# Kernel optimization log

Hardware: AMD Instinct MI355X
Metric: run time of the kernel (lower is better)

The kernel has to match this reference:

```python
import jax, jax.numpy as jnp
import numpy as np

NUM_HEADS = 4
NUM_EXPERTS = 8
TOP_K = 2
AUX_W = 0.1


def setup_inputs() -> dict:
    key = jax.random.key(0)
    ks = jax.random.split(key, 16)
    B, W, C, T = 32, 64, 27, 2000
    E_EEG, H, S = 200, 256, 768
    D2 = 2 * H  # MoE input/hidden dim = 512
    s = 0.02

    def p(k, shape):
        return (jax.random.normal(k, shape, jnp.float32) * s)

    z = lambda *shape: jnp.zeros(shape, jnp.float32)
    return {
        "eeg_windows": jax.random.normal(ks[0], (B, W, C, T), jnp.float32),
        "padding_mask": jnp.zeros((B, W), bool),
        "smiles_emb": jax.random.normal(ks[1], (B, S), jnp.float32),
        # window encoder (linear stand-in): flatten (C*T) -> E_EEG
        "enc_W": p(ks[2], (C * T, E_EEG)), "enc_b": z(E_EEG),
        # aggregator (masked-mean + linear stand-in): E_EEG -> H
        "agg_W": p(ks[3], (E_EEG, H)), "agg_b": z(H),
        # smiles projection
        "smiles_W": p(ks[4], (S, H)), "smiles_b": z(H),
        # cross attention
        "Wq": p(ks[5], (H, H)), "bq": z(H),
        "Wk": p(ks[6], (H, H)), "bk": z(H),
        "Wv": p(ks[7], (H, H)), "bv": z(H),
        "Wo": p(ks[8], (H, H)), "bo": z(H),
        # MoE gate + experts
        "gate_W": p(ks[9], (D2, NUM_EXPERTS)), "gate_b": z(NUM_EXPERTS),
        "exp_W1": p(ks[10], (NUM_EXPERTS, D2, D2)), "exp_b1": z(NUM_EXPERTS, D2),
        "exp_W2": p(ks[11], (NUM_EXPERTS, D2, H)), "exp_b2": z(NUM_EXPERTS, H),
        # classifier
        "ln_g": jnp.ones((H,), jnp.float32), "ln_b": z(H),
        "cls_W": p(ks[12], (H, 2)), "cls_b": z(2),
    }


def reference(eeg_windows, padding_mask, smiles_emb, enc_W, enc_b, agg_W, agg_b,
              smiles_W, smiles_b, Wq, bq, Wk, bk, Wv, bv, Wo, bo,
              gate_W, gate_b, exp_W1, exp_b1, exp_W2, exp_b2,
              ln_g, ln_b, cls_W, cls_b):
    B, W, C, T = eeg_windows.shape
    H = agg_W.shape[1]
    dh = H // NUM_HEADS

    # --- window encoding (stand-in linear encoder) ---
    wemb = eeg_windows.reshape(B, W, C * T) @ enc_W + enc_b  # (B, W, E_EEG)

    # --- aggregator: masked mean pool over windows, then project ---
    valid = (~padding_mask).astype(wemb.dtype)[..., None]      # (B, W, 1)
    pooled = (wemb * valid).sum(1) / jnp.maximum(valid.sum(1), 1.0)
    eeg_emb = pooled @ agg_W + agg_b                           # (B, H)

    smiles_proj = smiles_emb @ smiles_W + smiles_b             # (B, H)

    # --- cross attention (single query token over single kv token) ---
    q = (eeg_emb @ Wq + bq).reshape(B, NUM_HEADS, dh)
    k = (smiles_proj @ Wk + bk).reshape(B, NUM_HEADS, dh)
    v = (smiles_proj @ Wv + bv).reshape(B, NUM_HEADS, dh)
    scores = (q * k).sum(-1, keepdims=True) / jnp.sqrt(jnp.float32(dh))
    attn = jnp.exp(scores - scores)  # softmax over a single key == 1
    attended = (attn * v).reshape(B, H) @ Wo + bo              # (B, H)

    fused = jnp.concatenate([attended, smiles_proj], axis=-1)  # (B, 2H)

    # --- sparse MoE: dense experts, top-k gate, gather, combine ---
    gate_probs = jax.nn.softmax(fused @ gate_W + gate_b, axis=-1)  # (B, E)
    topk_p, topk_i = jax.lax.top_k(gate_probs, TOP_K)
    topk_p = topk_p / topk_p.sum(-1, keepdims=True)
    h1 = jax.nn.gelu(jnp.einsum('bd,edh->beh', fused, exp_W1) + exp_b1,
                     approximate=False)
    expert_out = jnp.einsum('beh,eho->beo', h1, exp_W2) + exp_b2   # (B, E, H)
    sel = jnp.take_along_axis(expert_out, topk_i[:, :, None], axis=1)
    moe_out = (sel * topk_p[..., None]).sum(1)                     # (B, H)

    usage = gate_probs.mean(0)
    uniform = jnp.ones_like(usage) / usage.shape[-1]
    aux = (usage * jnp.log(uniform) - jnp.log(usage) * uniform).sum()

    # --- classifier: LayerNorm + Linear ---
    mu = moe_out.mean(-1, keepdims=True)
    var = moe_out.var(-1, keepdims=True)
    xn = (moe_out - mu) / jnp.sqrt(var + 1e-5)
    logits = (xn * ln_g + ln_b) @ cls_W + cls_b                    # (B, 2)
    return logits, aux * AUX_W
```

## Files before the change

### kernel.cpp

```cpp
#include <hip/hip_runtime.h>
#include <math.h>

#define HD 256
#define SD 768
#define D2 512
#define NE 8
#define NB 32
#define NBLK 256
#define NTHR 256
#define SFP 516

typedef float f32x4 __attribute__((ext_vector_type(4)));
typedef unsigned u32x4 __attribute__((ext_vector_type(4)));

__device__ __forceinline__ float gelu_exact(float x) {
    return 0.5f * x * (1.0f + erff(x * 0.70710678118654752f));
}

__device__ __forceinline__ void cstf(float* p, float v) {
    __hip_atomic_store(p, v, __ATOMIC_RELAXED, __HIP_MEMORY_SCOPE_AGENT);
}
__device__ __forceinline__ float cldf(const float* p) {
    return __hip_atomic_load(p, __ATOMIC_RELAXED, __HIP_MEMORY_SCOPE_AGENT);
}
__device__ __forceinline__ void csti(int* p, int v) {
    __hip_atomic_store(p, v, __ATOMIC_RELAXED, __HIP_MEMORY_SCOPE_AGENT);
}
__device__ __forceinline__ int cldi(const int* p) {
    return __hip_atomic_load(p, __ATOMIC_RELAXED, __HIP_MEMORY_SCOPE_AGENT);
}

__device__ __forceinline__ void stage16k(const float* __restrict__ gsrc,
                                         float* __restrict__ lds, int t)
{
    const f32x4* src = (const f32x4*)gsrc;
    f32x4 r[16];
    #pragma unroll
    for (int j = 0; j < 16; ++j) {
        const f32x4* p = src + (t + j * 256);
        asm volatile("global_load_dwordx4 %0, %1, off sc0 sc1"
                     : "=v"(r[j]) : "v"(p));
    }
    asm volatile("s_waitcnt vmcnt(0)" ::: "memory");
    __builtin_amdgcn_sched_barrier(0);
    #pragma unroll
    for (int j = 0; j < 16; ++j) {
        int q = t + j * 256;
        *(f32x4*)&lds[(q >> 7) * SFP + (q & 127) * 4] = r[j];
    }
}

__device__ __forceinline__ void post_slot(unsigned* slots, unsigned tok) {
    __syncthreads();
    if (threadIdx.x == 0)
        __hip_atomic_store(slots + blockIdx.x, tok, __ATOMIC_RELAXED,
                           __HIP_MEMORY_SCOPE_AGENT);
}

__device__ __forceinline__ void wait_slots(const unsigned* slots, int nq,
                                           unsigned tok) {
    if (threadIdx.x < 64 && (int)threadIdx.x < nq) {
        const u32x4* p = (const u32x4*)slots + threadIdx.x;
        for (;;) {
            u32x4 v;
            asm volatile("global_load_dwordx4 %0, %1, off sc0 sc1\n\t"
                         "s_waitcnt vmcnt(0)"
                         : "=&v"(v) : "v"(p) : "memory");
            if ((v[0] == tok) & (v[1] == tok) & (v[2] == tok) & (v[3] == tok))
                break;
            __builtin_amdgcn_s_sleep(2);
        }
    }
    __builtin_amdgcn_fence(__ATOMIC_ACQUIRE, "workgroup");
    __syncthreads();
}

#define S_F     0
#define S_W     16512
#define S_R2    (16512 + 8192)
#define S_RED   (16512 + 8192 + 2048)
#define S_SMALL (16512 + 8192 + 2048 + 256)
#define SMEM_F  (16512 + 8192 + 2048 + 256 + 16)

__global__ __launch_bounds__(256) void fused_all(
    const float* __restrict__ smiles,
    const float* __restrict__ sW, const float* __restrict__ sb,
    const float* __restrict__ Wv, const float* __restrict__ bv,
    const float* __restrict__ Wo, const float* __restrict__ bo,
    const float* __restrict__ gW, const float* __restrict__ gb,
    const float* __restrict__ W1, const float* __restrict__ b1,
    const float* __restrict__ W2, const float* __restrict__ b2,
    const float* __restrict__ lng, const float* __restrict__ lnb,
    const float* __restrict__ clsW, const float* __restrict__ clsb,
    float* __restrict__ proj, float* __restrict__ fused,
    float* __restrict__ probs, float* __restrict__ pn,
    int* __restrict__ sel, float* __restrict__ h1,
    float* __restrict__ eo,
    unsigned* __restrict__ slot0, unsigned* __restrict__ slot1,
    unsigned* __restrict__ slot2, unsigned* __restrict__ slot3,
    unsigned* __restrict__ LC, float* __restrict__ out)
{
    __shared__ __align__(16) float smem[SMEM_F];
    __shared__ unsigned s_lc;
    const int bid = blockIdx.x, t = threadIdx.x;

    if (t == 0)
        s_lc = __hip_atomic_load(LC, __ATOMIC_RELAXED, __HIP_MEMORY_SCOPE_AGENT);
    __syncthreads();
    const unsigned tb = s_lc * 2654435761u;

    {
        int r = bid >> 3, sl = bid & 7;
        float* s_in = smem + S_F;
        float* s_red = smem + S_RED;
        const float* srow = smiles + (size_t)r * SD;
        for (int i = t; i < SD / 4; i += NTHR)
            ((float4*)s_in)[i] = ((const float4*)srow)[i];
        __syncthreads();
        int c = t & 31, kq = t >> 5;
        float acc = 0.f;
        const float* wp = sW + (size_t)(kq * 96) * HD + sl * 32 + c;
        #pragma unroll 8
        for (int k = 0; k < 96; ++k)
            acc = fmaf(s_in[kq * 96 + k], wp[(size_t)k * HD], acc);
        s_red[t] = acc;
        __syncthreads();
        if (t < 32) {
            float s = 0.f;
            #pragma unroll
            for (int q = 0; q < 8; ++q) s += s_red[q * 32 + t];
            int col = sl * 32 + t;
            s += sb[col];
            cstf(proj + r * HD + col, s);
            cstf(fused + (size_t)r * 2 * HD + HD + col, s);
        }
    }
    post_slot(slot0, tb + 1u);

    if (bid < NB) {
        wait_slots(slot0 + bid * 8, 2, tb + 1u);
        int b = bid;
        float* s_p   = smem + S_F;
        float* s_v   = smem + S_F + 256;
        float* s_f2  = smem + S_F + 512;
        float* s_acc = smem + S_R2;
        float* s_red = smem + S_RED;
        float* s_gate = smem + S_SMALL;
        s_p[t] = cldf(proj + b * HD + t);
        __syncthreads();
        int ks = t >> 6, cg = t & 63;

        f32x4 av = {0.f, 0.f, 0.f, 0.f};
        #pragma unroll 16
        for (int kk = 0; kk < 64; ++kk) {
            int k = ks * 64 + kk;
            f32x4 w = *(const f32x4*)(Wv + (size_t)k * HD + cg * 4);
            av += s_p[k] * w;
        }
        *(f32x4*)&s_acc[ks * 256 + cg * 4] = av;
        __syncthreads();
        s_v[t] = s_acc[t] + s_acc[256 + t] + s_acc[512 + t] + s_acc[768 + t]
               + bv[t];
        __syncthreads();

        f32x4 ao = {0.f, 0.f, 0.f, 0.f};
        #pragma unroll 16
        for (int kk = 0; kk < 64; ++kk) {
            int k = ks * 64 + kk;
            f32x4 w = *(const f32x4*)(Wo + (size_t)k * HD + cg * 4);
            ao += s_v[k] * w;
        }
        *(f32x4*)&s_acc[ks * 256 + cg * 4] = ao;
        __syncthreads();
        float att = s_acc[t] + s_acc[256 + t] + s_acc[512 + t] + s_acc[768 + t]
                  + bo[t];
        s_f2[t] = att;
        s_f2[HD + t] = s_p[t];
        cstf(fused + (size_t)b * 2 * HD + t, att);
        __syncthreads();

        int e = t & 7, ch = t >> 3;
        float gp = 0.f;
        #pragma unroll
        for (int j = 0; j < 16; ++j) {
            int d = ch * 16 + j;
            gp = fmaf(s_f2[d], gW[d * NE + e], gp);
        }
        s_red[t] = gp;
        __syncthreads();
        for (int off = 128; off >= 8; off >>= 1) {
            if (t < off) s_red[t] += s_red[t + off];
            __syncthreads();
        }
        if (t < NE) s_gate[t] = s_red[t] + gb[t];
        __syncthreads();
        if (t == 0) {
            float m = s_gate[0];
            for (int i = 1; i < NE; ++i) m = fmaxf(m, s_gate[i]);
            float ex[NE], ssum = 0.f;
            for (int i = 0; i < NE; ++i) { ex[i] = expf(s_gate[i] - m); ssum += ex[i]; }
            float pr[NE];
            for (int i = 0; i < NE; ++i) { pr[i] = ex[i] / ssum; cstf(probs + b * NE + i, pr[i]); }
            int i1 = 0;
            for (int i = 1; i < NE; ++i) if (pr[i] > pr[i1]) i1 = i;
            int i2 = (i1 == 0) ? 1 : 0;
            for (int i = 0; i < NE; ++i) if (i != i1 && pr[i] > pr[i2]) i2 = i;
            float p1 = pr[i1], p2 = pr[i2], s12 = p1 + p2;
            csti(sel + b * 2 + 0, i1);
            csti(sel + b * 2 + 1, i2);
            cstf(pn + b * 2 + 0, p1 / s12);
            cstf(pn + b * 2 + 1, p2 / s12);
        }
        post_slot(slot1, tb + 2u);
    }

    wait_slots(slot1, 8, tb + 2u);
    {
        int e = bid >> 5, ct = bid & 31;
        float* s_f  = smem + S_F;
        float* s_w  = smem + S_W;
        float* s_r2 = smem + S_R2;
        stage16k(fused, s_f, t);
        {
            const float* Wb = W1 + (size_t)e * D2 * D2 + ct * 16;
            #pragma unroll
            for (int j = 0; j < 8; ++j) {
                int q = t + j * 256;
                int k = q >> 2, c4 = (q & 3) * 4;
                *(float4*)&s_w[k * 16 + c4] =
                    *(const float4*)(Wb + (size_t)k * D2 + c4);
            }
        }
        __syncthreads();
        int ks = t >> 6, l = t & 63;
        int rp = l >> 2, c4g = l & 3;
        int r0 = rp * 2, r1 = r0 + 1;
        const float* fr0 = s_f + r0 * SFP;
        const float* fr1 = s_f + r1 * SFP;
        const float* wb = s_w + c4g * 4;
        f32x4 a0 = {0.f, 0.f, 0.f, 0.f}, a1 = {0.f, 0.f, 0.f, 0.f};
        #pragma unroll 4
        for (int kq = 0; kq < 32; ++kq) {
            int k = ks * 128 + kq * 4;
            f32x4 w0 = *(const f32x4*)&wb[(k + 0) * 16];
            f32x4 w1 = *(const f32x4*)&wb[(k + 1) * 16];
            f32x4 w2 = *(const f32x4*)&wb[(k + 2) * 16];
            f32x4 w3 = *(const f32x4*)&wb[(k + 3) * 16];
            f32x4 f0 = *(const f32x4*)&fr0[k];
            f32x4 f1 = *(const f32x4*)&fr1[k];
            a0 += f0[0] * w0 + f0[1] * w1 + f0[2] * w2 + f0[3] * w3;
            a1 += f1[0] * w0 + f1[1] * w1 + f1[2] * w2 + f1[3] * w3;
        }
        int cl = c4g * 4;
        #pragma unroll
        for (int j = 0; j < 4; ++j) {
            s_r2[(r0 * 16 + cl + j) * 4 + ks] = a0[j];
            s_r2[(r1 * 16 + cl + j) * 4 + ks] = a1[j];
        }
        __syncthreads();
        #pragma unroll
        for (int o = 0; o < 2; ++o) {
            int outi = t * 2 + o;
            f32x4 p = *(const f32x4*)&s_r2[outi * 4];
            int r = outi >> 4, cl2 = outi & 15;
            int col = ct * 16 + cl2;
            float v = p[0] + p[1] + p[2] + p[3] + b1[e * D2 + col];
            cstf(h1 + ((size_t)e * NB + r) * D2 + col, gelu_exact(v));
        }
    }
    post_slot(slot2, tb + 3u);
    if (bid >= 128) return;

    {
        int e = bid >> 4, ct = bid & 15;
        wait_slots(slot2 + e * 32, 8, tb + 3u);
        float* s_h  = smem + S_F;
        float* s_w  = smem + S_W;
        float* s_r2 = smem + S_R2;
        stage16k(h1 + (size_t)e * NB * D2, s_h, t);
        {
            const float* Wb = W2 + (size_t)e * D2 * HD + ct * 16;
            #pragma unroll
            for (int j = 0; j < 8; ++j) {
                int q = t + j * 256;
                int k = q >> 2, c4 = (q & 3) * 4;
                *(float4*)&s_w[k * 16 + c4] =
                    *(const float4*)(Wb + (size_t)k * HD + c4);
            }
        }
        __syncthreads();
        int ks = t >> 6, l = t & 63;
        int rp = l >> 2, c4g = l & 3;
        int r0 = rp * 2, r1 = r0 + 1;
        const float* fr0 = s_h + r0 * SFP;
        const float* fr1 = s_h + r1 * SFP;
        const float* wb = s_w + c4g * 4;
        f32x4 a0 = {0.f, 0.f, 0.f, 0.f}, a1 = {0.f, 0.f, 0.f, 0.f};
        #pragma unroll 4
        for (int kq = 0; kq < 32; ++kq) {
            int k = ks * 128 + kq * 4;
            f32x4 w0 = *(const f32x4*)&wb[(k + 0) * 16];
            f32x4 w1 = *(const f32x4*)&wb[(k + 1) * 16];
            f32x4 w2 = *(const f32x4*)&wb[(k + 2) * 16];
            f32x4 w3 = *(const f32x4*)&wb[(k + 3) * 16];
            f32x4 f0 = *(const f32x4*)&fr0[k];
            f32x4 f1 = *(const f32x4*)&fr1[k];
            a0 += f0[0] * w0 + f0[1] * w1 + f0[2] * w2 + f0[3] * w3;
            a1 += f1[0] * w0 + f1[1] * w1 + f1[2] * w2 + f1[3] * w3;
        }
        int cl = c4g * 4;
        #pragma unroll
        for (int j = 0; j < 4; ++j) {
            s_r2[(r0 * 16 + cl + j) * 4 + ks] = a0[j];
            s_r2[(r1 * 16 + cl + j) * 4 + ks] = a1[j];
        }
        __syncthreads();
        #pragma unroll
        for (int o = 0; o < 2; ++o) {
            int outi = t * 2 + o;
            f32x4 p = *(const f32x4*)&s_r2[outi * 4];
            int r = outi >> 4, cl2 = outi & 15;
            int col = ct * 16 + cl2;
            float v = p[0] + p[1] + p[2] + p[3] + b2[e * HD + col];
            cstf(eo + ((size_t)e * NB + r) * HD + col, v);
        }
    }
    post_slot(slot3, tb + 4u);
    if (bid >= NB) return;

    wait_slots(slot3, 32, tb + 4u);
    {
        int b = bid;
        float* s_red = smem + S_RED;
        float* s_stats = smem + S_SMALL;
        int e0 = cldi(sel + b * 2 + 0), e1 = cldi(sel + b * 2 + 1);
        float p0 = cldf(pn + b * 2 + 0), p1 = cldf(pn + b * 2 + 1);
        float moe = p0 * cldf(eo + ((size_t)e0 * NB + b) * HD + t)
                  + p1 * cldf(eo + ((size_t)e1 * NB + b) * HD + t);

        s_red[t] = moe; __syncthreads();
        for (int off = 128; off > 0; off >>= 1) {
            if (t < off) s_red[t] += s_red[t + off];
            __syncthreads();
        }
        if (t == 0) s_stats[0] = s_red[0] * (1.f / HD);
        __syncthreads();
        float mu = s_stats[0];
        float d = moe - mu;

        s_red[t] = d * d; __syncthreads();
        for (int off = 128; off > 0; off >>= 1) {
            if (t < off) s_red[t] += s_red[t + off];
            __syncthreads();
        }
        if (t == 0) s_stats[1] = s_red[0] * (1.f / HD);
        __syncthreads();

        float xn = d * rsqrtf(s_stats[1] + 1e-5f);
        float y = fmaf(xn, lng[t], lnb[t]);

        s_red[t] = y * clsW[t * 2 + 0]; __syncthreads();
        for (int off = 128; off > 0; off >>= 1) {
            if (t < off) s_red[t] += s_red[t + off];
            __syncthreads();
        }
        if (t == 0) s_stats[2] = s_red[0] + clsb[0];
        __syncthreads();

        s_red[t] = y * clsW[t * 2 + 1]; __syncthreads();
        for (int off = 128; off > 0; off >>= 1) {
            if (t < off) s_red[t] += s_red[t + off];
            __syncthreads();
        }
        if (t == 0) {
            out[b * 2 + 0] = s_stats[2];
            out[b * 2 + 1] = s_red[0] + clsb[1];
        }

        if (bid == 0) {
            __syncthreads();
            s_red[t] = cldf(probs + t);
            __syncthreads();
            for (int off = 128; off >= 8; off >>= 1) {
                if (t < off) s_red[t] += s_red[t + off];
                __syncthreads();
            }
            if (t == 0) {
                float aux = 0.f;
                for (int e = 0; e < NE; ++e) {
                    float u = s_red[e] * (1.f / 32.f);
                    aux += u * logf(0.125f) - logf(u) * 0.125f;
                }
                out[64] = 0.1f * aux;
            }
        }
    }

    if (bid == 0) {
        wait_slots(slot0, 64, tb + 1u);
        if (t == 0)
            __hip_atomic_store(LC, s_lc + 1u, __ATOMIC_RELAXED,
                               __HIP_MEMORY_SCOPE_AGENT);
    }
}

extern "C" void kernel_launch(void* const* d_in, const int* in_sizes, int n_in,
                              void* d_out, int out_size, void* d_ws, size_t ws_size,
                              hipStream_t stream) {
    (void)in_sizes; (void)n_in; (void)out_size; (void)ws_size;
    const float* smiles = (const float*)d_in[2];
    const float* sW  = (const float*)d_in[7];
    const float* sb  = (const float*)d_in[8];
    const float* Wv  = (const float*)d_in[13];
    const float* bv  = (const float*)d_in[14];
    const float* Wo  = (const float*)d_in[15];
    const float* bo  = (const float*)d_in[16];
    const float* gW  = (const float*)d_in[17];
    const float* gb  = (const float*)d_in[18];
    const float* W1  = (const float*)d_in[19];
    const float* b1  = (const float*)d_in[20];
    const float* W2  = (const float*)d_in[21];
    const float* b2  = (const float*)d_in[22];
    const float* lng = (const float*)d_in[23];
    const float* lnb = (const float*)d_in[24];
    const float* cW  = (const float*)d_in[25];
    const float* cb  = (const float*)d_in[26];
    float* out = (float*)d_out;
    float* ws  = (float*)d_ws;

    float*    proj  = ws;
    float*    fused = ws + 8192;
    float*    probs = ws + 24576;
    float*    pn    = ws + 24832;
    int*      sel   = (int*)(ws + 24896);
    float*    h1    = ws + 24960;
    float*    eo    = ws + 156032;
    unsigned* slot0 = (unsigned*)(ws + 221568);
    unsigned* slot1 = (unsigned*)(ws + 221824);
    unsigned* slot2 = (unsigned*)(ws + 221888);
    unsigned* slot3 = (unsigned*)(ws + 222144);
    unsigned* LC    = (unsigned*)(ws + 222272);

    fused_all<<<NBLK, NTHR, 0, stream>>>(
        smiles, sW, sb, Wv, bv, Wo, bo, gW, gb, W1, b1, W2, b2,
        lng, lnb, cW, cb,
        proj, fused, probs, pn, sel, h1, eo,
        slot0, slot1, slot2, slot3, LC, out);
}
```

Baseline: 44.01 us.

## Use leader-based grid barriers, prefetch expert weights before barriers, widen row tiling

Replaces the per-block polling of many slot entries with a barrier in which block 0 polls all slots and publishes a generation token that the other blocks spin on. All 256 blocks now post every slot. Expert W1/W2 weight tiles are loaded into shared memory before each barrier so the global loads overlap the wait. The expert GEMM inner loop changes from 2 rows by 4 k-splits to 4 rows by 8 k-splits, which needs a larger reduction buffer. The trade-off is an extra serial hop through the leader block on every barrier.

Result: faster. 38.82 us (-11.8%).

```diff
diff --git a/kernel.cpp b/kernel.cpp
--- a/kernel.cpp
+++ b/kernel.cpp
@@ -57,9 +57,40 @@
                            __HIP_MEMORY_SCOPE_AGENT);
 }
 
-__device__ __forceinline__ void wait_slots(const unsigned* slots, int nq,
-                                           unsigned tok) {
-    if (threadIdx.x < 64 && (int)threadIdx.x < nq) {
+__device__ __forceinline__ void finish_full(const unsigned* slots,
+                                            unsigned* gen, unsigned tok) {
+    const int t = threadIdx.x;
+    if (blockIdx.x == 0) {
+        if (t < 64) {
+            const u32x4* p = (const u32x4*)slots + t;
+            for (;;) {
+                u32x4 v;
+                asm volatile("global_load_dwordx4 %0, %1, off sc0 sc1\n\t"
+                             "s_waitcnt vmcnt(0)"
+                             : "=&v"(v) : "v"(p) : "memory");
+                bool ok = (v[0] == tok) & (v[1] == tok) &
+                          (v[2] == tok) & (v[3] == tok);
+                if (__ballot(ok) == ~0ull) break;
+                __builtin_amdgcn_s_sleep(1);
+            }
+            if (t == 0)
+                __hip_atomic_store(gen, tok, __ATOMIC_RELAXED,
+                                   __HIP_MEMORY_SCOPE_AGENT);
+        }
+    } else {
+        if (t == 0) {
+            while (__hip_atomic_load(gen, __ATOMIC_RELAXED,
+                                     __HIP_MEMORY_SCOPE_AGENT) != tok)
+                __builtin_amdgcn_s_sleep(1);
+        }
+    }
+    __builtin_amdgcn_fence(__ATOMIC_ACQUIRE, "workgroup");
+    __syncthreads();
+}
+
+__device__ __forceinline__ void wait_subset(const unsigned* slots, int nq,
+                                            unsigned tok) {
+    if ((int)threadIdx.x < nq) {
         const u32x4* p = (const u32x4*)slots + threadIdx.x;
         for (;;) {
             u32x4 v;
@@ -78,9 +109,9 @@
 #define S_F     0
 #define S_W     16512
 #define S_R2    (16512 + 8192)
-#define S_RED   (16512 + 8192 + 2048)
-#define S_SMALL (16512 + 8192 + 2048 + 256)
-#define SMEM_F  (16512 + 8192 + 2048 + 256 + 16)
+#define S_RED   (16512 + 8192 + 4096)
+#define S_SMALL (16512 + 8192 + 4096 + 256)
+#define SMEM_F  (16512 + 8192 + 4096 + 256 + 16)
 
 __global__ __launch_bounds__(256) void fused_all(
     const float* __restrict__ smiles,
@@ -98,7 +129,8 @@
     float* __restrict__ eo,
     unsigned* __restrict__ slot0, unsigned* __restrict__ slot1,
     unsigned* __restrict__ slot2, unsigned* __restrict__ slot3,
-    unsigned* __restrict__ LC, float* __restrict__ out)
+    unsigned* __restrict__ gen, unsigned* __restrict__ LC,
+    float* __restrict__ out)
 {
     __shared__ __align__(16) float smem[SMEM_F];
     __shared__ unsigned s_lc;
@@ -138,7 +170,7 @@
     post_slot(slot0, tb + 1u);
 
     if (bid < NB) {
-        wait_slots(slot0 + bid * 8, 2, tb + 1u);
+        wait_subset(slot0 + bid * 8, 2, tb + 1u);
         int b = bid;
         float* s_p   = smem + S_F;
         float* s_v   = smem + S_F + 256;
@@ -211,124 +243,136 @@
             cstf(pn + b * 2 + 0, p1 / s12);
             cstf(pn + b * 2 + 1, p2 / s12);
         }
-        post_slot(slot1, tb + 2u);
-    }
-
-    wait_slots(slot1, 8, tb + 2u);
+    }
+    post_slot(slot1, tb + 2u);
+
+    {
+        int e = bid >> 5, ct = bid & 31;
+        float* s_w = smem + S_W;
+        const float* Wb = W1 + (size_t)e * D2 * D2 + ct * 16;
+        #pragma unroll
+        for (int j = 0; j < 8; ++j) {
+            int q = t + j * 256;
+            int k = q >> 2, c4 = (q & 3) * 4;
+            *(float4*)&s_w[k * 16 + c4] = *(const float4*)(Wb + (size_t)k * D2 + c4);
+        }
+    }
+    finish_full(slot1, gen + 0, tb + 2u);
+
     {
         int e = bid >> 5, ct = bid & 31;
         float* s_f  = smem + S_F;
         float* s_w  = smem + S_W;
         float* s_r2 = smem + S_R2;
         stage16k(fused, s_f, t);
-        {
-            const float* Wb = W1 + (size_t)e * D2 * D2 + ct * 16;
-            #pragma unroll
-            for (int j = 0; j < 8; ++j) {
-                int q = t + j * 256;
-                int k = q >> 2, c4 = (q & 3) * 4;
-                *(float4*)&s_w[k * 16 + c4] =
-                    *(const float4*)(Wb + (size_t)k * D2 + c4);
-            }
-        }
-        __syncthreads();
-        int ks = t >> 6, l = t & 63;
-        int rp = l >> 2, c4g = l & 3;
-        int r0 = rp * 2, r1 = r0 + 1;
-        const float* fr0 = s_f + r0 * SFP;
-        const float* fr1 = s_f + r1 * SFP;
+        __syncthreads();
+        int ks = t >> 5, l = t & 31;
+        int rg = l >> 2, c4g = l & 3;
         const float* wb = s_w + c4g * 4;
-        f32x4 a0 = {0.f, 0.f, 0.f, 0.f}, a1 = {0.f, 0.f, 0.f, 0.f};
-        #pragma unroll 4
-        for (int kq = 0; kq < 32; ++kq) {
-            int k = ks * 128 + kq * 4;
+        int k0 = ks * 64;
+        f32x4 a0 = {0.f,0.f,0.f,0.f}, a1 = a0, a2 = a0, a3 = a0;
+        #pragma unroll 2
+        for (int kq = 0; kq < 16; ++kq) {
+            int k = k0 + kq * 4;
             f32x4 w0 = *(const f32x4*)&wb[(k + 0) * 16];
             f32x4 w1 = *(const f32x4*)&wb[(k + 1) * 16];
             f32x4 w2 = *(const f32x4*)&wb[(k + 2) * 16];
             f32x4 w3 = *(const f32x4*)&wb[(k + 3) * 16];
-            f32x4 f0 = *(const f32x4*)&fr0[k];
-            f32x4 f1 = *(const f32x4*)&fr1[k];
-            a0 += f0[0] * w0 + f0[1] * w1 + f0[2] * w2 + f0[3] * w3;
-            a1 += f1[0] * w0 + f1[1] * w1 + f1[2] * w2 + f1[3] * w3;
-        }
-        int cl = c4g * 4;
-        #pragma unroll
-        for (int j = 0; j < 4; ++j) {
-            s_r2[(r0 * 16 + cl + j) * 4 + ks] = a0[j];
-            s_r2[(r1 * 16 + cl + j) * 4 + ks] = a1[j];
-        }
+            f32x4 f0 = *(const f32x4*)&s_f[(rg     ) * SFP + k];
+            f32x4 f1 = *(const f32x4*)&s_f[(rg +  8) * SFP + k];
+            f32x4 f2 = *(const f32x4*)&s_f[(rg + 16) * SFP + k];
+            f32x4 f3 = *(const f32x4*)&s_f[(rg + 24) * SFP + k];
+            a0 += f0[0]*w0 + f0[1]*w1 + f0[2]*w2 + f0[3]*w3;
+            a1 += f1[0]*w0 + f1[1]*w1 + f1[2]*w2 + f1[3]*w3;
+            a2 += f2[0]*w0 + f2[1]*w1 + f2[2]*w2 + f2[3]*w3;
+            a3 += f3[0]*w0 + f3[1]*w1 + f3[2]*w2 + f3[3]*w3;
+        }
+        *(f32x4*)&s_r2[ks * 512 + (rg     ) * 16 + c4g * 4] = a0;
+        *(f32x4*)&s_r2[ks * 512 + (rg +  8) * 16 + c4g * 4] = a1;
+        *(f32x4*)&s_r2[ks * 512 + (rg + 16) * 16 + c4g * 4] = a2;
+        *(f32x4*)&s_r2[ks * 512 + (rg + 24) * 16 + c4g * 4] = a3;
         __syncthreads();
         #pragma unroll
         for (int o = 0; o < 2; ++o) {
             int outi = t * 2 + o;
-            f32x4 p = *(const f32x4*)&s_r2[outi * 4];
-            int r = outi >> 4, cl2 = outi & 15;
-            int col = ct * 16 + cl2;
-            float v = p[0] + p[1] + p[2] + p[3] + b1[e * D2 + col];
-            cstf(h1 + ((size_t)e * NB + r) * D2 + col, gelu_exact(v));
+            float s = 0.f;
+            #pragma unroll
+            for (int p = 0; p < 8; ++p) s += s_r2[p * 512 + outi];
+            int r = outi >> 4, cl = outi & 15;
+            int col = ct * 16 + cl;
+            cstf(h1 + ((size_t)e * NB + r) * D2 + col,
+                 gelu_exact(s + b1[e * D2 + col]));
         }
     }
     post_slot(slot2, tb + 3u);
-    if (bid >= 128) return;
+
+    if (bid >= 128) {
+        post_slot(slot3, tb + 4u);
+        return;
+    }
 
     {
         int e = bid >> 4, ct = bid & 15;
-        wait_slots(slot2 + e * 32, 8, tb + 3u);
-        float* s_h  = smem + S_F;
+        float* s_w = smem + S_W;
+        const float* Wb = W2 + (size_t)e * D2 * HD + ct * 16;
+        #pragma unroll
+        for (int j = 0; j < 8; ++j) {
+            int q = t + j * 256;
+            int k = q >> 2, c4 = (q & 3) * 4;
+            *(float4*)&s_w[k * 16 + c4] = *(const float4*)(Wb + (size_t)k * HD + c4);
+        }
+    }
+    finish_full(slot2, gen + 1, tb + 3u);
+
+    {
+        int e = bid >> 4, ct = bid & 15;
+        float* s_f  = smem + S_F;
         float* s_w  = smem + S_W;
         float* s_r2 = smem + S_R2;
-        stage16k(h1 + (size_t)e * NB * D2, s_h, t);
-        {
-            const float* Wb = W2 + (size_t)e * D2 * HD + ct * 16;
-            #pragma unroll
-            for (int j = 0; j < 8; ++j) {
-                int q = t + j * 256;
-                int k = q >> 2, c4 = (q & 3) * 4;
-                *(float4*)&s_w[k * 16 + c4] =
-                    *(const float4*)(Wb + (size_t)k * HD + c4);
-            }
-        }
-        __syncthreads();
-        int ks = t >> 6, l = t & 63;
-        int rp = l >> 2, c4g = l & 3;
-        int r0 = rp * 2, r1 = r0 + 1;
-        const float* fr0 = s_h + r0 * SFP;
-        const float* fr1 = s_h + r1 * SFP;
+        stage16k(h1 + (size_t)e * NB * D2, s_f, t);
+        __syncthreads();
+        int ks = t >> 5, l = t & 31;
+        int rg = l >> 2, c4g = l & 3;
         const float* wb = s_w + c4g * 4;
-        f32x4 a0 = {0.f, 0.f, 0.f, 0.f}, a1 = {0.f, 0.f, 0.f, 0.f};
-        #pragma unroll 4
-        for (int kq = 0; kq < 32; ++kq) {
-            int k = ks * 128 + kq * 4;
+        int k0 = ks * 64;
+        f32x4 a0 = {0.f,0.f,0.f,0.f}, a1 = a0, a2 = a0, a3 = a0;
+        #pragma unroll 2
+        for (int kq = 0; kq < 16; ++kq) {
+            int k = k0 + kq * 4;
             f32x4 w0 = *(const f32x4*)&wb[(k + 0) * 16];
             f32x4 w1 = *(const f32x4*)&wb[(k + 1) * 16];
             f32x4 w2 = *(const f32x4*)&wb[(k + 2) * 16];
             f32x4 w3 = *(const f32x4*)&wb[(k + 3) * 16];
-            f32x4 f0 = *(const f32x4*)&fr0[k];
-            f32x4 f1 = *(const f32x4*)&fr1[k];
-            a0 += f0[0] * w0 + f0[1] * w1 + f0[2] * w2 + f0[3] * w3;
-            a1 += f1[0] * w0 + f1[1] * w1 + f1[2] * w2 + f1[3] * w3;
-        }
-        int cl = c4g * 4;
-        #pragma unroll
-        for (int j = 0; j < 4; ++j) {
-            s_r2[(r0 * 16 + cl + j) * 4 + ks] = a0[j];
-            s_r2[(r1 * 16 + cl + j) * 4 + ks] = a1[j];
-        }
+            f32x4 f0 = *(const f32x4*)&s_f[(rg     ) * SFP + k];
+            f32x4 f1 = *(const f32x4*)&s_f[(rg +  8) * SFP + k];
+            f32x4 f2 = *(const f32x4*)&s_f[(rg + 16) * SFP + k];
+            f32x4 f3 = *(const f32x4*)&s_f[(rg + 24) * SFP + k];
+            a0 += f0[0]*w0 + f0[1]*w1 + f0[2]*w2 + f0[3]*w3;
+            a1 += f1[0]*w0 + f1[1]*w1 + f1[2]*w2 + f1[3]*w3;
+            a2 += f2[0]*w0 + f2[1]*w1 + f2[2]*w2 + f2[3]*w3;
+            a3 += f3[0]*w0 + f3[1]*w1 + f3[2]*w2 + f3[3]*w3;
+        }
+        *(f32x4*)&s_r2[ks * 512 + (rg     ) * 16 + c4g * 4] = a0;
+        *(f32x4*)&s_r2[ks * 512 + (rg +  8) * 16 + c4g * 4] = a1;
+        *(f32x4*)&s_r2[ks * 512 + (rg + 16) * 16 + c4g * 4] = a2;
+        *(f32x4*)&s_r2[ks * 512 + (rg + 24) * 16 + c4g * 4] = a3;
         __syncthreads();
         #pragma unroll
         for (int o = 0; o < 2; ++o) {
             int outi = t * 2 + o;
-            f32x4 p = *(const f32x4*)&s_r2[outi * 4];
-            int r = outi >> 4, cl2 = outi & 15;
-            int col = ct * 16 + cl2;
-            float v = p[0] + p[1] + p[2] + p[3] + b2[e * HD + col];
-            cstf(eo + ((size_t)e * NB + r) * HD + col, v);
+            float s = 0.f;
+            #pragma unroll
+            for (int p = 0; p < 8; ++p) s += s_r2[p * 512 + outi];
+            int r = outi >> 4, cl = outi & 15;
+            int col = ct * 16 + cl;
+            cstf(eo + ((size_t)e * NB + r) * HD + col, s + b2[e * HD + col]);
         }
     }
     post_slot(slot3, tb + 4u);
     if (bid >= NB) return;
 
-    wait_slots(slot3, 32, tb + 4u);
+    finish_full(slot3, gen + 2, tb + 4u);
+
     {
         int b = bid;
         float* s_red = smem + S_RED;
@@ -396,12 +440,9 @@
         }
     }
 
-    if (bid == 0) {
-        wait_slots(slot0, 64, tb + 1u);
-        if (t == 0)
-            __hip_atomic_store(LC, s_lc + 1u, __ATOMIC_RELAXED,
-                               __HIP_MEMORY_SCOPE_AGENT);
-    }
+    if (bid == 0 && t == 0)
+        __hip_atomic_store(LC, s_lc + 1u, __ATOMIC_RELAXED,
+                           __HIP_MEMORY_SCOPE_AGENT);
 }
 
 extern "C" void kernel_launch(void* const* d_in, const int* in_sizes, int n_in,
@@ -437,13 +478,14 @@
     float*    eo    = ws + 156032;
     unsigned* slot0 = (unsigned*)(ws + 221568);
     unsigned* slot1 = (unsigned*)(ws + 221824);
-    unsigned* slot2 = (unsigned*)(ws + 221888);
-    unsigned* slot3 = (unsigned*)(ws + 222144);
-    unsigned* LC    = (unsigned*)(ws + 222272);
+    unsigned* slot2 = (unsigned*)(ws + 222080);
+    unsigned* slot3 = (unsigned*)(ws + 222336);
+    unsigned* gen   = (unsigned*)(ws + 222592);
+    unsigned* LC    = (unsigned*)(ws + 222596);
 
     fused_all<<<NBLK, NTHR, 0, stream>>>(
         smiles, sW, sb, Wv, bv, Wo, bo, gW, gb, W1, b1, W2, b2,
         lng, lnb, cW, cb,
         proj, fused, probs, pn, sel, h1, eo,
-        slot0, slot1, slot2, slot3, LC, out);
-}
+        slot0, slot1, slot2, slot3, gen, LC, out);
+}
```
